# Performance work log

Measured on AMD Instinct MI355X. Metric: run time of the kernel, lower is better.

The kernel has to match this reference:

```python
import jax, jax.numpy as jnp
import numpy as np

B, T, D, F, C = 16384, 256, 8, 512, 16  # batch, trees, depth, features, classes
L = 2 ** D  # leaves per tree


def setup_inputs() -> dict:
    key = jax.random.key(0)
    k1, k2, k3, k4 = jax.random.split(key, 4)
    x = jax.random.normal(k1, (B, F), dtype=jnp.float32)
    feature_weights = jax.random.normal(k2, (T, D, F), dtype=jnp.float32)
    thresholds = jax.random.normal(k3, (T, D), dtype=jnp.float32)
    responses = jax.random.normal(k4, (T, L, C), dtype=jnp.float32)
    return {"x": x, "feature_weights": feature_weights,
            "thresholds": thresholds, "responses": responses}


def reference(x, feature_weights, thresholds, responses):
    # Hard feature selection per (tree, level): argmax over features.
    fidx = jnp.argmax(feature_weights, axis=-1)            # [T, D] int
    fv = x[:, fidx]                                        # [B, T, D] gather
    bits = (fv > thresholds[None, :, :]).astype(x.dtype)   # [B, T, D]
    # decision = sum_d bit_d * 2^(D-1-d)  (matches decision*2+bit loop)
    powers = (2 ** jnp.arange(D - 1, -1, -1)).astype(x.dtype)  # [D]
    decision = jnp.sum(bits * powers, axis=-1).astype(jnp.int32)  # [B, T]
    # Gather leaf responses per (sample, tree) and average over trees.
    tree_ids = jnp.arange(T)[None, :]                      # [1, T]
    leaf_out = responses[tree_ids, decision]               # [B, T, C]
    out = jnp.mean(leaf_out, axis=1)                       # [B, C]
    return out  # dropout is identity at eval time
```

## Files before the change

### kernel.cpp

```cpp
#include <hip/hip_runtime.h>

constexpr int B = 16384;
constexpr int T = 256;
constexpr int D = 8;
constexpr int F = 512;
constexpr int C = 16;
constexpr int L = 256;

typedef float f32x4 __attribute__((ext_vector_type(4)));

struct FP { int fidx; float thr; };

__device__ __forceinline__ unsigned int bf16_rne(float f) {
    const unsigned int u = __float_as_uint(f);
    return (u + 0x7fffu + ((u >> 16) & 1u)) >> 16;
}

__global__ __launch_bounds__(256) void prep_kernel(
    const float* __restrict__ fw,
    const float* __restrict__ thr,
    const float* __restrict__ resp,
    FP* __restrict__ packed,
    unsigned int* __restrict__ rb)
{
    if (blockIdx.x < 512) {
        const int wave = threadIdx.x >> 6;
        const int lane = threadIdx.x & 63;
        const int row  = blockIdx.x * 4 + wave;
        const float* base = fw + (size_t)row * F;

        float best = -INFINITY;
        int bidx = 0;
#pragma unroll
        for (int k = 0; k < F / 64; ++k) {
            const int idx = lane + k * 64;
            const float v = base[idx];
            if (v > best) { best = v; bidx = idx; }
        }
#pragma unroll
        for (int off = 32; off >= 1; off >>= 1) {
            const float ov = __shfl_xor(best, off);
            const int   oi = __shfl_xor(bidx, off);
            if (ov > best || (ov == best && oi < bidx)) { best = ov; bidx = oi; }
        }
        if (lane == 0) {
            FP p;
            p.fidx = bidx;
            p.thr  = thr[row];
            packed[row] = p;
        }
    } else {
        const int i = (blockIdx.x - 512) * 256 + threadIdx.x;
        const float4* s = reinterpret_cast<const float4*>(resp) + i * 2;
        const float4 a = s[0], b = s[1];
        uint4 o;
        o.x = bf16_rne(a.x) | (bf16_rne(a.y) << 16);
        o.y = bf16_rne(a.z) | (bf16_rne(a.w) << 16);
        o.z = bf16_rne(b.x) | (bf16_rne(b.y) << 16);
        o.w = bf16_rne(b.z) | (bf16_rne(b.w) << 16);
        reinterpret_cast<uint4*>(rb)[i] = o;
    }
}

__global__ __launch_bounds__(256, 4) void forest_kernel(
    const float* __restrict__ x,
    const FP* __restrict__ packed,
    const unsigned short* __restrict__ rb,
    float* __restrict__ out)
{
    __shared__ float xrow[4][F];
    __shared__ unsigned char sdec[4][T];

    const int b0  = blockIdx.x * 4;
    const int tid = threadIdx.x;

    {
        const float4* xs = reinterpret_cast<const float4*>(x + (size_t)b0 * F);
        float4* xl = reinterpret_cast<float4*>(&xrow[0][0]);
        xl[tid]       = xs[tid];
        xl[tid + 256] = xs[tid + 256];
    }
    __syncthreads();

    {
        const int2* p2 = reinterpret_cast<const int2*>(packed) + tid * D;
        int2 raw[D];
#pragma unroll
        for (int d = 0; d < D; ++d) raw[d] = p2[d];
        int dec0 = 0, dec1 = 0, dec2 = 0, dec3 = 0;
#pragma unroll
        for (int d = 0; d < D; ++d) {
            const int   f  = raw[d].x;
            const float th = __int_as_float(raw[d].y);
            const int   p  = 128 >> d;
            dec0 |= (xrow[0][f] > th) ? p : 0;
            dec1 |= (xrow[1][f] > th) ? p : 0;
            dec2 |= (xrow[2][f] > th) ? p : 0;
            dec3 |= (xrow[3][f] > th) ? p : 0;
        }
        sdec[0][tid] = (unsigned char)dec0;
        sdec[1][tid] = (unsigned char)dec1;
        sdec[2][tid] = (unsigned char)dec2;
        sdec[3][tid] = (unsigned char)dec3;
    }
    __syncthreads();

    const int w    = tid >> 6;
    const int lane = tid & 63;

    const int* pw  = reinterpret_cast<const int*>(&sdec[w][0]);
    const int wsel = lane >> 4;
    const int bsel = ((lane >> 2) & 3) * 8;
    const int lbase = ((lane >> 2) << 12) | ((lane & 3) << 2);

    int dw[16];
#pragma unroll
    for (int kk = 0; kk < 16; ++kk) dw[kk] = pw[4 * kk + wsel];

    uint2 r[16];
#pragma unroll
    for (int kk = 0; kk < 16; ++kk) {
        const int dd = (dw[kk] >> bsel) & 255;
        r[kk] = *reinterpret_cast<const uint2*>(rb + (kk << 16) + (dd << 4) + lbase);
    }

    float4 acc = make_float4(0.f, 0.f, 0.f, 0.f);
#pragma unroll
    for (int kk = 0; kk < 16; ++kk) {
        acc.x += __uint_as_float(r[kk].x << 16);
        acc.y += __uint_as_float(r[kk].x & 0xffff0000u);
        acc.z += __uint_as_float(r[kk].y << 16);
        acc.w += __uint_as_float(r[kk].y & 0xffff0000u);
    }

#pragma unroll
    for (int off = 4; off <= 32; off <<= 1) {
        acc.x += __shfl_xor(acc.x, off);
        acc.y += __shfl_xor(acc.y, off);
        acc.z += __shfl_xor(acc.z, off);
        acc.w += __shfl_xor(acc.w, off);
    }

    if (lane < 4) {
        const float sc = 1.0f / T;
        f32x4 o = { acc.x * sc, acc.y * sc, acc.z * sc, acc.w * sc };
        *reinterpret_cast<f32x4*>(out + ((size_t)(b0 + w) << 4) + (lane << 2)) = o;
    }
}

extern "C" void kernel_launch(void* const* d_in, const int* in_sizes, int n_in,
                              void* d_out, int out_size, void* d_ws, size_t ws_size,
                              hipStream_t stream) {
    const float* x         = (const float*)d_in[0];
    const float* fw        = (const float*)d_in[1];
    const float* thr       = (const float*)d_in[2];
    const float* responses = (const float*)d_in[3];
    float* out             = (float*)d_out;

    FP* packed        = (FP*)d_ws;
    unsigned int* rb  = (unsigned int*)((char*)d_ws + (1 << 16));

    prep_kernel<<<1024, 256, 0, stream>>>(fw, thr, responses, packed, rb);
    forest_kernel<<<B / 4, 256, 0, stream>>>(x, packed,
                                             (const unsigned short*)rb, out);
}
```

Measured before the change: 101.7 us.

## Stage tree params in LDS and compute decisions per wave, distributing via shuffles

Instead of each thread computing the decisions for one tree across all four rows and writing them to shared bytes, the block now stages the packed (feature, threshold) table in LDS. Each wave computes decisions for its own row, four trees per lane, and hands them out with cross-lane shuffles. This removes one block barrier and the byte-sized decision buffer. In exchange it adds 16 KB of LDS per block, which can reduce occupancy, and it adds shuffle traffic.

```diff
diff --git a/kernel.cpp b/kernel.cpp
--- a/kernel.cpp
+++ b/kernel.cpp
@@ -69,7 +69,7 @@
     float* __restrict__ out)
 {
     __shared__ float xrow[4][F];
-    __shared__ unsigned char sdec[4][T];
+    __shared__ int2  tbl[D][T];
 
     const int b0  = blockIdx.x * 4;
     const int tid = threadIdx.x;
@@ -80,42 +80,43 @@
         xl[tid]       = xs[tid];
         xl[tid + 256] = xs[tid + 256];
     }
-    __syncthreads();
-
     {
-        const int2* p2 = reinterpret_cast<const int2*>(packed) + tid * D;
-        int2 raw[D];
-#pragma unroll
-        for (int d = 0; d < D; ++d) raw[d] = p2[d];
-        int dec0 = 0, dec1 = 0, dec2 = 0, dec3 = 0;
-#pragma unroll
-        for (int d = 0; d < D; ++d) {
-            const int   f  = raw[d].x;
-            const float th = __int_as_float(raw[d].y);
-            const int   p  = 128 >> d;
-            dec0 |= (xrow[0][f] > th) ? p : 0;
-            dec1 |= (xrow[1][f] > th) ? p : 0;
-            dec2 |= (xrow[2][f] > th) ? p : 0;
-            dec3 |= (xrow[3][f] > th) ? p : 0;
-        }
-        sdec[0][tid] = (unsigned char)dec0;
-        sdec[1][tid] = (unsigned char)dec1;
-        sdec[2][tid] = (unsigned char)dec2;
-        sdec[3][tid] = (unsigned char)dec3;
+        const int4* tp = reinterpret_cast<const int4*>(packed + (size_t)tid * D);
+        const int4 q0 = tp[0], q1 = tp[1], q2 = tp[2], q3 = tp[3];
+        tbl[0][tid] = make_int2(q0.x, q0.y);
+        tbl[1][tid] = make_int2(q0.z, q0.w);
+        tbl[2][tid] = make_int2(q1.x, q1.y);
+        tbl[3][tid] = make_int2(q1.z, q1.w);
+        tbl[4][tid] = make_int2(q2.x, q2.y);
+        tbl[5][tid] = make_int2(q2.z, q2.w);
+        tbl[6][tid] = make_int2(q3.x, q3.y);
+        tbl[7][tid] = make_int2(q3.z, q3.w);
     }
     __syncthreads();
 
     const int w    = tid >> 6;
     const int lane = tid & 63;
 
-    const int* pw  = reinterpret_cast<const int*>(&sdec[w][0]);
-    const int wsel = lane >> 4;
+    const float* xb = &xrow[w][0];
+    unsigned int dec = 0;
+#pragma unroll
+    for (int d = 0; d < D; ++d) {
+        const int4 a = *reinterpret_cast<const int4*>(&tbl[d][4 * lane]);
+        const int4 b = *reinterpret_cast<const int4*>(&tbl[d][4 * lane + 2]);
+        const unsigned int bit = 128u >> d;
+        if (xb[a.x] > __int_as_float(a.y)) dec |= bit;
+        if (xb[a.z] > __int_as_float(a.w)) dec |= bit << 8;
+        if (xb[b.x] > __int_as_float(b.y)) dec |= bit << 16;
+        if (xb[b.z] > __int_as_float(b.w)) dec |= bit << 24;
+    }
+
+    const int src  = lane >> 4;
     const int bsel = ((lane >> 2) & 3) * 8;
-    const int lbase = ((lane >> 2) << 12) | ((lane & 3) << 2);
-
     int dw[16];
 #pragma unroll
-    for (int kk = 0; kk < 16; ++kk) dw[kk] = pw[4 * kk + wsel];
+    for (int kk = 0; kk < 16; ++kk) dw[kk] = __shfl((int)dec, 4 * kk + src);
+
+    const int lbase = ((lane >> 2) << 12) | ((lane & 3) << 2);
 
     uint2 r[16];
 #pragma unroll
```

Result: no change. 100.8 us (-0.8%).
